# Optimization experiments

Measured on AMD Instinct MI355X. Metric: run time of the kernel, lower is better.

## Reference

```python
import jax, jax.numpy as jnp
import numpy as np

# ---- q_config constants (from init_kwargs) ----
DIN_W, DIN_EW = 8, 4
DIN_P = (1, 32)
HASH_W = 8
DOUT_W, DOUT_EW = 8, 4
DOUT_P = (1, 32)


def reshape_to_block(x, t1, t0, p1, p0):
    # [..., t1, t0] -> [N, t1//p1, t0//p0, p1, p0]
    x = x.reshape(-1, t1 // p1, p1, t0 // p0, p0)
    return x.transpose(0, 1, 3, 2, 4)


def reshape_back(x, t1, t0, p1, p0):
    # [N, t1//p1, t0//p0, p1, p0] -> [N, t1, t0]
    return x.transpose(0, 1, 3, 2, 4).reshape(-1, t1, t0)


def _integer_quantize(x, width, frac_width):
    scale = 2.0 ** frac_width
    imin = -(2.0 ** (width - 1))
    imax = 2.0 ** (width - 1) - 1.0
    return jnp.clip(jnp.round(x * scale), imin, imax) / scale


def mxint_hardware(x, width, exponent_width, p1, p0):
    """Microscaling quantize: shared per-block exponent + signed int mantissa.
    Returns (dequantized qx [orig shape], mantissa mx [orig shape], exponent ex [N,T1,T0])."""
    orig_shape = x.shape
    t1, t0 = orig_shape[-2], orig_shape[-1]
    xb = reshape_to_block(x, t1, t0, p1, p0)            # [N,T1,T0,p1,p0]
    amax = jnp.max(jnp.abs(xb), axis=(-2, -1))          # [N,T1,T0]
    emax = 2.0 ** (exponent_width - 1) - 1.0
    emin = -(2.0 ** (exponent_width - 1))
    ex = jnp.clip(jnp.floor(jnp.log2(jnp.maximum(amax, 2.0 ** emin))), emin, emax)
    mscale = 2.0 ** (width - 1)
    scale = mscale / 2.0 ** ex[..., None, None]
    mb = jnp.clip(jnp.round(xb * scale), -mscale, mscale - 1.0)
    qb = mb / scale
    qx = reshape_back(qb, t1, t0, p1, p0).reshape(orig_shape)
    mx = reshape_back(mb, t1, t0, p1, p0).reshape(orig_shape)
    return qx, mx, ex


def mxint_gelu(x):
    qx, mx, ex = mxint_hardware(x, DIN_W, DIN_EW, *DIN_P)
    original_shape = qx.shape
    t1, t0 = mx.shape[-2], mx.shape[-1]
    p1, p0 = DIN_P
    qxb = reshape_to_block(qx, t1, t0, p1, p0)          # [N,T1,T0,p1,p0]
    exb = ex[..., None, None]                           # [N,T1,T0,1,1]
    qout = jax.nn.relu(qxb)
    remaining = (qxb > -3.0) & (qxb < 3.0)
    HW = HASH_W
    HFW = HW - 3
    # exact (erf-based) GELU, quantized to the hash-table output format
    qgelu = _integer_quantize(jax.nn.gelu(qxb, approximate=False), HW, HFW)
    # exponent-aligned requantization (torch float // is floor-division)
    mgelu = jnp.floor(qgelu * 2.0 ** (HW - 1) / 2.0 ** exb)
    qgelu = mgelu * 2.0 ** exb / 2.0 ** (HW - 1)
    qout = jnp.where(remaining, qgelu, qout)
    qout = reshape_back(qout, t1, t0, p1, p0).reshape(original_shape)
    qy, _, _ = mxint_hardware(qout, DOUT_W, DOUT_EW, *DOUT_P)
    return qy


def setup_inputs() -> dict:
    key = jax.random.key(0)
    x = jax.random.normal(key, (4, 2048, 4096), dtype=jnp.float32)
    return {"x": x}


def reference(x):
    return mxint_gelu(x)
```

## Files before the change

### kernel.cpp

```cpp
#include <hip/hip_runtime.h>
#include <cmath>


__device__ __forceinline__ float pow2i(int k) {
    union { unsigned u; float f; } c;
    c.u = (unsigned)(127 + k) << 23;
    return c.f;
}

__device__ __forceinline__ int block_exp(float amax) {
    int e = ilogbf(fmaxf(amax, 0x1p-8f));
    return max(-8, min(7, e));
}

__global__ __launch_bounds__(256) void build_lut_kernel(float* __restrict__ lut) {
    const int idx = blockIdx.x * 256 + threadIdx.x;
    const int e = (idx >> 8) - 8;
    const int m = (idx & 255) - 128;
    const float q = (float)m * pow2i(e - 7);
    float r = fmaxf(q, 0.f);
    if (q > -3.f && q < 3.f) {
        const float t = q / 1.41421356237309504880f;
        const float er = (float)erf((double)t);
        const float g = q * (er + 1.f) * 0.5f;
        float qg = rintf(g * 32.f);
        qg = fminf(fmaxf(qg, -128.f), 127.f);
        const float qgelu = qg * 0.03125f;
        const float mg = floorf(qgelu * pow2i(7 - e));
        r = mg * pow2i(e - 7);
    }
    lut[idx] = r;
}

__global__ __launch_bounds__(256) void mxint_gelu_lut_kernel(
    const float* __restrict__ in, float* __restrict__ out,
    const float* __restrict__ glut, unsigned n8)
{
    __shared__ float lut[4096];
    {
        const float4* g4 = reinterpret_cast<const float4*>(glut);
        float4* l4 = reinterpret_cast<float4*>(lut);
        #pragma unroll
        for (int k = 0; k < 4; ++k)
            l4[threadIdx.x + 256 * k] = g4[threadIdx.x + 256 * k];
    }
    __syncthreads();

    const unsigned stride = gridDim.x * 256u;
    for (unsigned u = blockIdx.x * 256u + threadIdx.x; u < n8; u += stride) {
        const float4* p = reinterpret_cast<const float4*>(in) + 2 * (size_t)u;
        const float4 va = p[0], vb = p[1];
        float x[8] = {va.x, va.y, va.z, va.w, vb.x, vb.y, vb.z, vb.w};

        float amax = 0.f;
        #pragma unroll
        for (int j = 0; j < 8; ++j) amax = fmaxf(amax, fabsf(x[j]));
        amax = fmaxf(amax, __shfl_xor(amax, 1, 64));
        amax = fmaxf(amax, __shfl_xor(amax, 2, 64));

        const int ex1 = block_exp(amax);
        const float s1 = pow2i(7 - ex1);
        const int base = (ex1 + 8) * 256 + 128;

        float o[8];
        float oamax = 0.f;
        #pragma unroll
        for (int j = 0; j < 8; ++j) {
            float m = rintf(x[j] * s1);
            m = fminf(fmaxf(m, -128.f), 127.f);
            const float r = lut[base + (int)m];
            o[j] = r;
            oamax = fmaxf(oamax, fabsf(r));
        }

        oamax = fmaxf(oamax, __shfl_xor(oamax, 1, 64));
        oamax = fmaxf(oamax, __shfl_xor(oamax, 2, 64));
        const int ex2 = block_exp(oamax);
        const float s2 = pow2i(7 - ex2);
        const float is2 = pow2i(ex2 - 7);

        float y[8];
        #pragma unroll
        for (int j = 0; j < 8; ++j) {
            float m = rintf(o[j] * s2);
            m = fminf(fmaxf(m, -128.f), 127.f);
            y[j] = m * is2;
        }
        float4* q = reinterpret_cast<float4*>(out) + 2 * (size_t)u;
        q[0] = make_float4(y[0], y[1], y[2], y[3]);
        q[1] = make_float4(y[4], y[5], y[6], y[7]);
    }
}

__global__ __launch_bounds__(256) void mxint_gelu_direct_kernel(
    const float* __restrict__ in, float* __restrict__ out, unsigned n4)
{
    unsigned i = blockIdx.x * 256u + threadIdx.x;
    if (i >= n4) return;
    const float4 xv = reinterpret_cast<const float4*>(in)[i];
    float x[4] = {xv.x, xv.y, xv.z, xv.w};
    float amax = fmaxf(fmaxf(fabsf(x[0]), fabsf(x[1])),
                       fmaxf(fabsf(x[2]), fabsf(x[3])));
    amax = fmaxf(amax, __shfl_xor(amax, 1, 64));
    amax = fmaxf(amax, __shfl_xor(amax, 2, 64));
    amax = fmaxf(amax, __shfl_xor(amax, 4, 64));
    const int ex1 = block_exp(amax);
    const float s1 = pow2i(7 - ex1), is1 = pow2i(ex1 - 7);
    float o[4]; float oamax = 0.f;
    #pragma unroll
    for (int j = 0; j < 4; ++j) {
        float m = rintf(x[j] * s1);
        m = fminf(fmaxf(m, -128.f), 127.f);
        const float q = m * is1;
        float r = fmaxf(q, 0.f);
        if (q > -3.f && q < 3.f) {
            const float t = q / 1.41421356237309504880f;
            const float e = (float)erf((double)t);
            const float g = q * (e + 1.f) * 0.5f;
            float qg = rintf(g * 32.f);
            qg = fminf(fmaxf(qg, -128.f), 127.f);
            const float mg = floorf(qg * 0.03125f * s1);
            r = mg * is1;
        }
        o[j] = r; oamax = fmaxf(oamax, fabsf(r));
    }
    oamax = fmaxf(oamax, __shfl_xor(oamax, 1, 64));
    oamax = fmaxf(oamax, __shfl_xor(oamax, 2, 64));
    oamax = fmaxf(oamax, __shfl_xor(oamax, 4, 64));
    const int ex2 = block_exp(oamax);
    const float s2 = pow2i(7 - ex2), is2 = pow2i(ex2 - 7);
    float y[4];
    #pragma unroll
    for (int j = 0; j < 4; ++j) {
        float m = rintf(o[j] * s2);
        m = fminf(fmaxf(m, -128.f), 127.f);
        y[j] = m * is2;
    }
    reinterpret_cast<float4*>(out)[i] =
        make_float4(y[0], y[1], y[2], y[3]);
}

extern "C" void kernel_launch(void* const* d_in, const int* in_sizes, int n_in,
                              void* d_out, int out_size, void* d_ws, size_t ws_size,
                              hipStream_t stream) {
    const float* x = (const float*)d_in[0];
    float* y = (float*)d_out;
    const unsigned n = (unsigned)in_sizes[0];

    if (ws_size >= 4096 * sizeof(float) && (n % 8u) == 0u) {
        float* lut = (float*)d_ws;
        build_lut_kernel<<<16, 256, 0, stream>>>(lut);
        const unsigned n8 = n / 8;
        unsigned blocks = 2048;
        if (blocks * 256u > n8) blocks = (n8 + 255u) / 256u;
        mxint_gelu_lut_kernel<<<blocks, 256, 0, stream>>>(x, y, lut, n8);
    } else {
        const unsigned n4 = n / 4;
        mxint_gelu_direct_kernel<<<(n4 + 255u) / 256u, 256, 0, stream>>>(x, y, n4);
    }
}
```

Before: 50.93 us.

## Process 16 elements per thread with register prefetch and nontemporal stores

Each thread now handles 16 contiguous floats instead of 8, so a 32-element block spans two lanes and needs one shuffle instead of two. The grid-stride loop loads the next iteration's four float4s into registers before computing the current one, software-pipelining global loads against LUT lookups. Output is written with nontemporal stores to avoid polluting cache. The cost is higher register pressure and fewer iterations per thread to overlap, since total work per grid stays the same.

Measured after the change: 194.5 us. 282% more time.

```diff
diff --git a/kernel.cpp b/kernel.cpp
--- a/kernel.cpp
+++ b/kernel.cpp
@@ -1,6 +1,8 @@
 #include <hip/hip_runtime.h>
 #include <cmath>
 
+
+typedef float floatx4 __attribute__((ext_vector_type(4)));
 
 __device__ __forceinline__ float pow2i(int k) {
     union { unsigned u; float f; } c;
@@ -34,12 +36,12 @@
 
 __global__ __launch_bounds__(256) void mxint_gelu_lut_kernel(
     const float* __restrict__ in, float* __restrict__ out,
-    const float* __restrict__ glut, unsigned n8)
+    const float* __restrict__ glut, unsigned n16)
 {
     __shared__ float lut[4096];
     {
-        const float4* g4 = reinterpret_cast<const float4*>(glut);
-        float4* l4 = reinterpret_cast<float4*>(lut);
+        const floatx4* g4 = reinterpret_cast<const floatx4*>(glut);
+        floatx4* l4 = reinterpret_cast<floatx4*>(lut);
         #pragma unroll
         for (int k = 0; k < 4; ++k)
             l4[threadIdx.x + 256 * k] = g4[threadIdx.x + 256 * k];
@@ -47,25 +49,44 @@
     __syncthreads();
 
     const unsigned stride = gridDim.x * 256u;
-    for (unsigned u = blockIdx.x * 256u + threadIdx.x; u < n8; u += stride) {
-        const float4* p = reinterpret_cast<const float4*>(in) + 2 * (size_t)u;
-        const float4 va = p[0], vb = p[1];
-        float x[8] = {va.x, va.y, va.z, va.w, vb.x, vb.y, vb.z, vb.w};
+    unsigned u = blockIdx.x * 256u + threadIdx.x;
+
+    floatx4 cur[4];
+    bool have = (u < n16);
+    if (have) {
+        const floatx4* p = reinterpret_cast<const floatx4*>(in) + 4 * (size_t)u;
+        cur[0] = p[0]; cur[1] = p[1]; cur[2] = p[2]; cur[3] = p[3];
+    }
+
+    while (have) {
+        const unsigned un = u + stride;
+        floatx4 nxt[4];
+        const bool have_n = (un < n16);
+        if (have_n) {
+            const floatx4* p = reinterpret_cast<const floatx4*>(in) + 4 * (size_t)un;
+            nxt[0] = p[0]; nxt[1] = p[1]; nxt[2] = p[2]; nxt[3] = p[3];
+        }
+
+        float x[16];
+        #pragma unroll
+        for (int k = 0; k < 4; ++k) {
+            x[4*k+0] = cur[k].x; x[4*k+1] = cur[k].y;
+            x[4*k+2] = cur[k].z; x[4*k+3] = cur[k].w;
+        }
 
         float amax = 0.f;
         #pragma unroll
-        for (int j = 0; j < 8; ++j) amax = fmaxf(amax, fabsf(x[j]));
+        for (int j = 0; j < 16; ++j) amax = fmaxf(amax, fabsf(x[j]));
         amax = fmaxf(amax, __shfl_xor(amax, 1, 64));
-        amax = fmaxf(amax, __shfl_xor(amax, 2, 64));
 
         const int ex1 = block_exp(amax);
         const float s1 = pow2i(7 - ex1);
         const int base = (ex1 + 8) * 256 + 128;
 
-        float o[8];
+        float o[16];
         float oamax = 0.f;
         #pragma unroll
-        for (int j = 0; j < 8; ++j) {
+        for (int j = 0; j < 16; ++j) {
             float m = rintf(x[j] * s1);
             m = fminf(fmaxf(m, -128.f), 127.f);
             const float r = lut[base + (int)m];
@@ -74,21 +95,26 @@
         }
 
         oamax = fmaxf(oamax, __shfl_xor(oamax, 1, 64));
-        oamax = fmaxf(oamax, __shfl_xor(oamax, 2, 64));
         const int ex2 = block_exp(oamax);
         const float s2 = pow2i(7 - ex2);
         const float is2 = pow2i(ex2 - 7);
 
-        float y[8];
+        floatx4* q = reinterpret_cast<floatx4*>(out) + 4 * (size_t)u;
         #pragma unroll
-        for (int j = 0; j < 8; ++j) {
-            float m = rintf(o[j] * s2);
-            m = fminf(fmaxf(m, -128.f), 127.f);
-            y[j] = m * is2;
+        for (int k = 0; k < 4; ++k) {
+            floatx4 yv;
+            float m0 = fminf(fmaxf(rintf(o[4*k+0] * s2), -128.f), 127.f);
+            float m1 = fminf(fmaxf(rintf(o[4*k+1] * s2), -128.f), 127.f);
+            float m2 = fminf(fmaxf(rintf(o[4*k+2] * s2), -128.f), 127.f);
+            float m3 = fminf(fmaxf(rintf(o[4*k+3] * s2), -128.f), 127.f);
+            yv.x = m0 * is2; yv.y = m1 * is2; yv.z = m2 * is2; yv.w = m3 * is2;
+            __builtin_nontemporal_store(yv, q + k);
         }
-        float4* q = reinterpret_cast<float4*>(out) + 2 * (size_t)u;
-        q[0] = make_float4(y[0], y[1], y[2], y[3]);
-        q[1] = make_float4(y[4], y[5], y[6], y[7]);
+
+        #pragma unroll
+        for (int k = 0; k < 4; ++k) cur[k] = nxt[k];
+        u = un;
+        have = have_n;
     }
 }
 
@@ -147,13 +173,13 @@
     float* y = (float*)d_out;
     const unsigned n = (unsigned)in_sizes[0];
 
-    if (ws_size >= 4096 * sizeof(float) && (n % 8u) == 0u) {
+    if (ws_size >= 4096 * sizeof(float) && (n % 32u) == 0u) {
         float* lut = (float*)d_ws;
         build_lut_kernel<<<16, 256, 0, stream>>>(lut);
-        const unsigned n8 = n / 8;
+        const unsigned n16 = n / 16;
         unsigned blocks = 2048;
-        if (blocks * 256u > n8) blocks = (n8 + 255u) / 256u;
-        mxint_gelu_lut_kernel<<<blocks, 256, 0, stream>>>(x, y, lut, n8);
+        if (blocks * 256u > n16) blocks = (n16 + 255u) / 256u;
+        mxint_gelu_lut_kernel<<<blocks, 256, 0, stream>>>(x, y, lut, n16);
     } else {
         const unsigned n4 = n / 4;
         mxint_gelu_direct_kernel<<<(n4 + 255u) / 256u, 256, 0, stream>>>(x, y, n4);
```
